# Optimization experiments

Hardware: AMD Instinct MI355X
Metric: run time of the kernel (lower is better)

The kernel has to match this reference:

```python
import jax, jax.numpy as jnp
import numpy as np

K = 3   # spatial_kernel_size
M = 5   # memory_size


def setup_inputs() -> dict:
    key = jax.random.key(0)
    ks = jax.random.split(key, 16)
    C = 64
    B, H, D, W = 2, 24, 24, 24
    s = 0.05
    n = jax.random.normal
    return {
        "x": n(ks[0], (B, C, H, D, W), jnp.float32),
        "prev_memory": jnp.zeros((B, C), jnp.float32),
        "Wq": n(ks[1], (C, C), jnp.float32) * s,
        "bq": n(ks[2], (C,), jnp.float32) * s,
        "Wk": n(ks[3], (C, C), jnp.float32) * s,
        "bk": n(ks[4], (C,), jnp.float32) * s,
        "Wv": n(ks[5], (C, C), jnp.float32) * s,
        "bv": n(ks[6], (C,), jnp.float32) * s,
        "mem_key": n(ks[7], (C, M), jnp.float32),
        "mem_value": n(ks[8], (C, M), jnp.float32),
        "Wg": n(ks[9], (C, 2 * C), jnp.float32) * s,
        "bg": n(ks[10], (C,), jnp.float32) * s,
        "W_ih": n(ks[11], (3 * C, C), jnp.float32) * s,
        "W_hh": n(ks[12], (3 * C, C), jnp.float32) * s,
        "b_ih": n(ks[13], (3 * C,), jnp.float32) * s,
        "b_hh": n(ks[14], (3 * C,), jnp.float32) * s,
    }


def _patches(x, k):
    # x: (B,C,H,D,W) -> (B,C,k^3,H,D,W) local neighborhoods (zero-padded)
    B, C, H, D, W = x.shape
    p = k // 2
    xp = jnp.pad(x, ((0, 0), (0, 0), (p, p), (p, p), (p, p)))
    sl = [xp[:, :, i:i + H, j:j + D, l:l + W]
          for i in range(k) for j in range(k) for l in range(k)]
    return jnp.stack(sl, axis=2)


def reference(x, prev_memory, Wq, bq, Wk, bk, Wv, bv, mem_key, mem_value,
              Wg, bg, W_ih, W_hh, b_ih, b_hh):
    B, C, H, D, W = x.shape
    N = H * D * W
    xf = x.reshape(B, C, N)
    pf = _patches(x, K).reshape(B, C, K ** 3, N)

    # 1x1x1 conv projections (pure channel mixes)
    q = jnp.einsum('oc,bcn->bon', Wq, xf) + bq[None, :, None]            # (B,C,N)
    k_sp = jnp.einsum('oc,bcmn->bomn', Wk, pf) + bk[None, :, None, None]  # (B,C,27,N)
    v_sp = jnp.einsum('oc,bcmn->bomn', Wv, pf) + bv[None, :, None, None]

    # memory tokens broadcast over all spatial locations
    k_mem = jnp.broadcast_to(mem_key[None, :, :, None], (B, C, M, N))
    v_mem = jnp.broadcast_to(mem_value[None, :, :, None], (B, C, M, N))
    kk = jnp.concatenate([k_mem, k_sp], axis=2)   # (B,C,M+27,N)
    vv = jnp.concatenate([v_mem, v_sp], axis=2)

    # per-channel scalar attention over memory+neighborhood axis
    attn = jax.nn.softmax(q[:, :, None, :] * kk / jnp.sqrt(jnp.float32(C)), axis=2)
    out = jnp.sum(attn * vv, axis=2).reshape(B, C, H, D, W)

    # sigmoid gate over concat([x, out])
    gin = jnp.concatenate([xf, out.reshape(B, C, N)], axis=1)  # (B,2C,N)
    gate = jax.nn.sigmoid(jnp.einsum('oc,bcn->bon', Wg, gin)
                          + bg[None, :, None]).reshape(B, C, H, D, W)
    out = gate * out + (1.0 - gate) * x

    # GRU memory update on spatially pooled features (torch GRUCell math)
    mu = out.mean(axis=(2, 3, 4))                 # (B,C)
    gi = mu @ W_ih.T + b_ih
    gh = prev_memory @ W_hh.T + b_hh
    ir, iz, ii = jnp.split(gi, 3, axis=1)
    hr, hz, hn = jnp.split(gh, 3, axis=1)
    r = jax.nn.sigmoid(ir + hr)
    z = jax.nn.sigmoid(iz + hz)
    ng = jnp.tanh(ii + r * hn)
    new_memory = (1.0 - z) * ng + z * prev_memory
    return out, new_memory
```

## Files before the change

### kernel.cpp

```cpp
#include <hip/hip_runtime.h>
#include <math.h>

#define NPOS 13824
#define CDIM 64
#define BTCH 2
#define LOG2E 1.4426950408889634f
#define QSCALE (0.125f * LOG2E)

__device__ __forceinline__ unsigned int f2bf1(float f) {
  unsigned int u = __float_as_uint(f);
  return (u + 0x7FFFu + ((u >> 16) & 1u)) >> 16;
}

__global__ __launch_bounds__(256) void qkvg_kernel(
    const float* __restrict__ x,
    const float* __restrict__ Wq, const float* __restrict__ bq,
    const float* __restrict__ Wk, const float* __restrict__ bk,
    const float* __restrict__ Wv, const float* __restrict__ bv,
    const float* __restrict__ Wg,
    float* __restrict__ Qb, float* __restrict__ Kb, float* __restrict__ Vb,
    float* __restrict__ GXT, float* __restrict__ pool)
{
  __shared__ __align__(16) float wqt[64*68];
  __shared__ __align__(16) float wkt[64*68];
  __shared__ __align__(16) float wvt[64*68];
  __shared__ __align__(16) float wgt[64*68];
  const int t  = threadIdx.x;
  const int bi = blockIdx.x;
  const int b  = bi / 216;
  const int n0 = (bi - b*216) * 64;
  if (bi == 0 && t < 128) pool[t] = 0.0f;

  #pragma unroll
  for (int k = 0; k < 16; ++k) {
    int idx = t + k*256;
    int lo = idx & 63, hi = idx >> 6;
    wqt[lo*68 + hi] = Wq[idx] * QSCALE;
    wkt[lo*68 + hi] = Wk[idx];
    wvt[lo*68 + hi] = Wv[idx];
    wgt[lo*68 + hi] = Wg[hi*128 + lo];
  }
  __syncthreads();

  const int c0  = (t & 15) * 4;
  const int nn0 = (t >> 4) * 4;
  const float* xbase = x + (size_t)(b*64)*NPOS + n0 + nn0;
  float aq[4][4] = {}; float ak[4][4] = {}; float av[4][4] = {}; float ag[4][4] = {};
  #pragma unroll 4
  for (int cp = 0; cp < 64; ++cp) {
    const float4 xv4 = *(const float4*)(xbase + (size_t)cp*NPOS);
    const float4 q4  = *(const float4*)&wqt[cp*68 + c0];
    const float4 k4  = *(const float4*)&wkt[cp*68 + c0];
    const float4 v4  = *(const float4*)&wvt[cp*68 + c0];
    const float4 g4  = *(const float4*)&wgt[cp*68 + c0];
    const float xa[4] = {xv4.x, xv4.y, xv4.z, xv4.w};
    const float qa[4] = {q4.x, q4.y, q4.z, q4.w};
    const float ka[4] = {k4.x, k4.y, k4.z, k4.w};
    const float va[4] = {v4.x, v4.y, v4.z, v4.w};
    const float ga[4] = {g4.x, g4.y, g4.z, g4.w};
    #pragma unroll
    for (int ci = 0; ci < 4; ++ci)
      #pragma unroll
      for (int ni = 0; ni < 4; ++ni) {
        aq[ci][ni] = fmaf(qa[ci], xa[ni], aq[ci][ni]);
        ak[ci][ni] = fmaf(ka[ci], xa[ni], ak[ci][ni]);
        av[ci][ni] = fmaf(va[ci], xa[ni], av[ci][ni]);
        ag[ci][ni] = fmaf(ga[ci], xa[ni], ag[ci][ni]);
      }
  }
  float4 xr[4];
  #pragma unroll
  for (int e = 0; e < 4; ++e)
    xr[e] = *(const float4*)(x + (size_t)(b*64 + c0 + e)*NPOS + n0 + nn0);
  const float xre[4][4] = {{xr[0].x,xr[0].y,xr[0].z,xr[0].w},
                           {xr[1].x,xr[1].y,xr[1].z,xr[1].w},
                           {xr[2].x,xr[2].y,xr[2].z,xr[2].w},
                           {xr[3].x,xr[3].y,xr[3].z,xr[3].w}};
  const float4 bq4 = *(const float4*)&bq[c0];
  const float4 bk4 = *(const float4*)&bk[c0];
  const float4 bv4 = *(const float4*)&bv[c0];
  #pragma unroll
  for (int ni = 0; ni < 4; ++ni) {
    const int p = b*NPOS + n0 + nn0 + ni;
    float4 o;
    o = make_float4(fmaf(bq4.x,QSCALE,aq[0][ni]), fmaf(bq4.y,QSCALE,aq[1][ni]),
                    fmaf(bq4.z,QSCALE,aq[2][ni]), fmaf(bq4.w,QSCALE,aq[3][ni]));
    *(float4*)&Qb[p*64 + c0] = o;
    o = make_float4(ak[0][ni]+bk4.x, ak[1][ni]+bk4.y, ak[2][ni]+bk4.z, ak[3][ni]+bk4.w);
    *(float4*)&Kb[p*64 + c0] = o;
    o = make_float4(av[0][ni]+bv4.x, av[1][ni]+bv4.y, av[2][ni]+bv4.z, av[3][ni]+bv4.w);
    *(float4*)&Vb[p*64 + c0] = o;
    o = make_float4(ag[0][ni], xre[0][ni], ag[1][ni], xre[1][ni]);
    *(float4*)&GXT[(size_t)(p*64 + c0)*2]     = o;
    o = make_float4(ag[2][ni], xre[2][ni], ag[3][ni], xre[3][ni]);
    *(float4*)&GXT[(size_t)(p*64 + c0)*2 + 4] = o;
  }
}

__global__ __launch_bounds__(256, 4) void attn_kernel(
    float* __restrict__ QOT,
    const float* __restrict__ Kb, const float* __restrict__ Vb,
    const float* __restrict__ GXT,
    const float* __restrict__ bk, const float* __restrict__ bv,
    const float* __restrict__ memk, const float* __restrict__ memv,
    const float* __restrict__ Wg, const float* __restrict__ bg,
    float* __restrict__ pool)
{
  __shared__ __align__(16) unsigned int kvbuf[8000];
  __shared__ __align__(16) float als[256];
  const int t = threadIdx.x;
  const int c = t & 63;
  const int w = t >> 6;

  {
    float* wgt2 = (float*)kvbuf;
    #pragma unroll
    for (int k = 0; k < 16; ++k) {
      int u = t + k*256;
      int cp = u >> 6, j = u & 63;
      wgt2[j*65 + cp] = Wg[cp*128 + 64 + j];
    }
  }
  __syncthreads();
  unsigned int wg2p[32];
  {
    const float* wgt2 = (const float*)kvbuf;
    #pragma unroll
    for (int j2 = 0; j2 < 32; ++j2) {
      unsigned lo = f2bf1(wgt2[(2*j2)*65 + c]);
      unsigned hi = f2bf1(wgt2[(2*j2+1)*65 + c]);
      wg2p[j2] = lo | (hi << 16);
    }
  }
  float mk[5], mv[5];
  #pragma unroll
  for (int m = 0; m < 5; ++m) { mk[m] = memk[c*5 + m]; mv[m] = memv[c*5 + m]; }
  const float bg_c = bg[c];
  __syncthreads();

  const int bi = (int)(blockIdx.x & 7) * 128 + (int)(blockIdx.x >> 3);
  const int b  = bi >> 9;
  const int tb = bi & 511;
  const int h0 = (tb >> 6) * 3;
  const int d0 = ((tb >> 3) & 7) * 3;
  const int w0 = (tb & 7) * 3;
  const int bN = b * NPOS;

  for (int u = t; u < 125*16; u += 256) {
    int pos = u >> 4, q4 = u & 15;
    int ph = pos / 25, pr = pos - ph*25;
    int pd = pr / 5,  pw = pr - pd*5;
    int hh = h0 - 1 + ph, dd = d0 - 1 + pd, ww = w0 - 1 + pw;
    bool inb = ((unsigned)hh < 24u) && ((unsigned)dd < 24u) && ((unsigned)ww < 24u);
    float4 kf, vf;
    if (inb) {
      const size_t off = ((size_t)(bN + hh*576 + dd*24 + ww))*64 + q4*4;
      kf = *(const float4*)(Kb + off);
      vf = *(const float4*)(Vb + off);
    } else {
      kf = ((const float4*)bk)[q4];
      vf = ((const float4*)bv)[q4];
    }
    uint4 pk;
    pk.x = (f2bf1(kf.x) << 16) | f2bf1(vf.x);
    pk.y = (f2bf1(kf.y) << 16) | f2bf1(vf.y);
    pk.z = (f2bf1(kf.z) << 16) | f2bf1(vf.z);
    pk.w = (f2bf1(kf.w) << 16) | f2bf1(vf.w);
    *(uint4*)&kvbuf[pos*64 + q4*4] = pk;
  }
  __syncthreads();

  float pacc = 0.0f;
  int li = w;
  int lh = li / 9, lr = li - lh*9, ld = lr / 3, lw = lr - ld*3;
  int p  = bN + (h0+lh)*576 + (d0+ld)*24 + (w0+lw);
  int hb = (lh*25 + ld*5 + lw)*64 + c;
  float q2 = QOT[p*64 + c];
  for (; li < 27; li += 4) {
    const int li_n = li + 4;
    int p_n = p, hb_n = hb;
    if (li_n < 27) {
      const int lh2 = li_n / 9, lr2 = li_n - lh2*9;
      const int ld2 = lr2 / 3,  lw2 = lr2 - ld2*3;
      p_n  = bN + (h0+lh2)*576 + (d0+ld2)*24 + (w0+lw2);
      hb_n = (lh2*25 + ld2*5 + lw2)*64 + c;
    }
    const float q_n = QOT[p_n*64 + c];
    const float2 gx = *(const float2*)&GXT[(size_t)(p*64 + c)*2];

    const unsigned int* kvp = &kvbuf[hb];
    unsigned int kvreg[27];
    #pragma unroll
    for (int i = 0; i < 3; ++i)
      #pragma unroll
      for (int j = 0; j < 3; ++j)
        #pragma unroll
        for (int l = 0; l < 3; ++l)
          kvreg[i*9 + j*3 + l] = kvp[(i*25 + j*5 + l)*64];
    float mx0 = q2*mk[0], mx1 = q2*mk[1], mx2 = q2*mk[2], mx3 = q2*mk[3];
    mx0 = fmaxf(mx0, q2*mk[4]);
    #pragma unroll
    for (int s = 0; s < 27; ++s) {
      float kf = __uint_as_float(kvreg[s] & 0xFFFF0000u);
      float lv = q2 * kf;
      if ((s & 3) == 0) mx0 = fmaxf(mx0, lv);
      else if ((s & 3) == 1) mx1 = fmaxf(mx1, lv);
      else if ((s & 3) == 2) mx2 = fmaxf(mx2, lv);
      else mx3 = fmaxf(mx3, lv);
    }
    const float maxv = fmaxf(fmaxf(mx0, mx1), fmaxf(mx2, mx3));

    float s0 = 0.f, s1 = 0.f, o0 = 0.f, o1 = 0.f;
    #pragma unroll
    for (int m = 0; m < 5; ++m) {
      float pf = __builtin_amdgcn_exp2f(fmaf(q2, mk[m], -maxv));
      if (m & 1) { s1 += pf; o1 = fmaf(pf, mv[m], o1); }
      else       { s0 += pf; o0 = fmaf(pf, mv[m], o0); }
    }
    #pragma unroll
    for (int s = 0; s < 27; ++s) {
      unsigned int kv = kvreg[s];
      float kf = __uint_as_float(kv & 0xFFFF0000u);
      float vf = __uint_as_float(kv << 16);
      float pf = __builtin_amdgcn_exp2f(fmaf(q2, kf, -maxv));
      if (s & 1) { s1 += pf; o1 = fmaf(pf, vf, o1); }
      else       { s0 += pf; o0 = fmaf(pf, vf, o0); }
    }
    const float att = (o0 + o1) * __builtin_amdgcn_rcpf(s0 + s1);

    als[w*64 + c] = att;
    float g0 = gx.x + bg_c, g1 = 0.f, g2 = 0.f, g3 = 0.f;
    #pragma unroll
    for (int j4 = 0; j4 < 16; ++j4) {
      const float4 a4 = *(const float4*)&als[w*64 + j4*4];
      const unsigned pk0 = wg2p[2*j4], pk1 = wg2p[2*j4+1];
      g0 = fmaf(__uint_as_float(pk0 << 16),         a4.x, g0);
      g1 = fmaf(__uint_as_float(pk0 & 0xFFFF0000u), a4.y, g1);
      g2 = fmaf(__uint_as_float(pk1 << 16),         a4.z, g2);
      g3 = fmaf(__uint_as_float(pk1 & 0xFFFF0000u), a4.w, g3);
    }
    const float gl   = (g0 + g1) + (g2 + g3);
    const float gate = __builtin_amdgcn_rcpf(1.0f + __builtin_amdgcn_exp2f(-LOG2E * gl));
    const float fin  = fmaf(gate, att - gx.y, gx.y);
    QOT[p*64 + c] = fin;
    pacc += fin;

    p = p_n; hb = hb_n; q2 = q_n;
  }

  als[t] = pacc;
  __syncthreads();
  if (t < 64) {
    float s = als[t] + als[64 + t] + als[128 + t] + als[192 + t];
    atomicAdd(&pool[b*64 + t], s);
  }
}

__global__ __launch_bounds__(256) void outpool_kernel(
    const float* __restrict__ OT, float* __restrict__ out,
    const float* __restrict__ pool, const float* __restrict__ prev,
    const float* __restrict__ W_ih, const float* __restrict__ W_hh,
    const float* __restrict__ b_ih, const float* __restrict__ b_hh,
    float* __restrict__ outmem)
{
  __shared__ __align__(16) float ls[64*65];
  __shared__ __align__(16) float mu[128];
  __shared__ float gi[384];
  __shared__ float gh[384];
  const int t  = threadIdx.x;
  const int bi = blockIdx.x;
  const int b  = bi / 216;
  const int n0 = (bi - b*216) * 64;
  #pragma unroll
  for (int i = 0; i < 16; ++i) {
    int u = i*256 + t;
    int pos = u >> 6, cc = u & 63;
    ls[cc*65 + pos] = OT[(size_t)(b*NPOS + n0 + pos)*64 + cc];
  }
  if (bi == 0 && t < 128) mu[t] = pool[t] * (1.0f / (float)NPOS);
  __syncthreads();
  #pragma unroll
  for (int i = 0; i < 16; ++i) {
    int u = i*256 + t;
    int cc = u >> 6, j = u & 63;
    out[(size_t)(b*64 + cc)*NPOS + n0 + j] = ls[cc*65 + j];
  }
  if (bi != 0) return;

  for (int r = t; r < 384; r += 256) {
    const int b2 = r / 192, j = r - b2*192;
    const float4* wi4 = (const float4*)(W_ih + (size_t)j*64);
    const float4* wh4 = (const float4*)(W_hh + (size_t)j*64);
    const float4* mu4 = (const float4*)(mu + b2*64);
    const float4* pv4 = (const float4*)(prev + b2*64);
    float sgi = b_ih[j], sgh = b_hh[j];
    #pragma unroll
    for (int k = 0; k < 16; ++k) {
      float4 wv = wi4[k], m4 = mu4[k];
      sgi = fmaf(wv.x, m4.x, sgi); sgi = fmaf(wv.y, m4.y, sgi);
      sgi = fmaf(wv.z, m4.z, sgi); sgi = fmaf(wv.w, m4.w, sgi);
      float4 hv = wh4[k], p4 = pv4[k];
      sgh = fmaf(hv.x, p4.x, sgh); sgh = fmaf(hv.y, p4.y, sgh);
      sgh = fmaf(hv.z, p4.z, sgh); sgh = fmaf(hv.w, p4.w, sgh);
    }
    gi[r] = sgi; gh[r] = sgh;
  }
  __syncthreads();
  if (t < 128) {
    const int b2 = t >> 6, cc = t & 63;
    float ir = gi[b2*192 + cc],       hr = gh[b2*192 + cc];
    float iz = gi[b2*192 + 64 + cc],  hz = gh[b2*192 + 64 + cc];
    float ii = gi[b2*192 + 128 + cc], hn = gh[b2*192 + 128 + cc];
    float rr = 1.0f / (1.0f + __builtin_amdgcn_exp2f(-LOG2E * (ir + hr)));
    float zz = 1.0f / (1.0f + __builtin_amdgcn_exp2f(-LOG2E * (iz + hz)));
    float ng = tanhf(ii + rr * hn);
    outmem[t] = (1.0f - zz) * ng + zz * prev[t];
  }
}

extern "C" void kernel_launch(void* const* d_in, const int* in_sizes, int n_in,
                              void* d_out, int out_size, void* d_ws, size_t ws_size,
                              hipStream_t stream) {
  const float* x    = (const float*)d_in[0];
  const float* prev = (const float*)d_in[1];
  const float* Wq   = (const float*)d_in[2];
  const float* bq   = (const float*)d_in[3];
  const float* Wk   = (const float*)d_in[4];
  const float* bk   = (const float*)d_in[5];
  const float* Wv   = (const float*)d_in[6];
  const float* bv   = (const float*)d_in[7];
  const float* memk = (const float*)d_in[8];
  const float* memv = (const float*)d_in[9];
  const float* Wg   = (const float*)d_in[10];
  const float* bg   = (const float*)d_in[11];
  const float* W_ih = (const float*)d_in[12];
  const float* W_hh = (const float*)d_in[13];
  const float* b_ih = (const float*)d_in[14];
  const float* b_hh = (const float*)d_in[15];

  float* out    = (float*)d_out;
  float* outmem = out + (size_t)BTCH*CDIM*NPOS;

  const size_t SZ = (size_t)BTCH*NPOS*CDIM;
  float* wsf  = (float*)d_ws;
  float* Qb   = wsf;
  float* Kb   = wsf + SZ;
  float* Vb   = wsf + 2*SZ;
  float* GXT  = wsf + 3*SZ;
  float* pool = wsf + 5*SZ;

  qkvg_kernel<<<BTCH*216, 256, 0, stream>>>(x, Wq, bq, Wk, bk, Wv, bv, Wg,
                                            Qb, Kb, Vb, GXT, pool);
  attn_kernel<<<BTCH*512, 256, 0, stream>>>(Qb, Kb, Vb, GXT,
                                            bk, bv, memk, memv, Wg, bg, pool);
  outpool_kernel<<<BTCH*216, 256, 0, stream>>>(Qb, out, pool, prev,
                                               W_ih, W_hh, b_ih, b_hh, outmem);
}
```

Before: 169.4 us.

## Store packed bf16 K/V from projection, drop softmax max pass, process two positions per iteration

The projection kernel now writes K and V as one packed bf16 buffer instead of two fp32 buffers, which halves the intermediate write traffic and the attention kernel's halo loads. The attention kernel no longer computes a running max before the exponentials, which relies on the scaled logits staying small enough not to overflow. Each thread now handles two output positions per loop iteration, interleaving their exp and gate work for more instruction-level parallelism. The cost is higher register pressure and a possible loss of numerical safety for large logits.

```diff
diff --git a/kernel.cpp b/kernel.cpp
--- a/kernel.cpp
+++ b/kernel.cpp
@@ -18,7 +18,7 @@
     const float* __restrict__ Wk, const float* __restrict__ bk,
     const float* __restrict__ Wv, const float* __restrict__ bv,
     const float* __restrict__ Wg,
-    float* __restrict__ Qb, float* __restrict__ Kb, float* __restrict__ Vb,
+    float* __restrict__ Qb, unsigned int* __restrict__ KVp,
     float* __restrict__ GXT, float* __restrict__ pool)
 {
   __shared__ __align__(16) float wqt[64*68];
@@ -86,10 +86,12 @@
     o = make_float4(fmaf(bq4.x,QSCALE,aq[0][ni]), fmaf(bq4.y,QSCALE,aq[1][ni]),
                     fmaf(bq4.z,QSCALE,aq[2][ni]), fmaf(bq4.w,QSCALE,aq[3][ni]));
     *(float4*)&Qb[p*64 + c0] = o;
-    o = make_float4(ak[0][ni]+bk4.x, ak[1][ni]+bk4.y, ak[2][ni]+bk4.z, ak[3][ni]+bk4.w);
-    *(float4*)&Kb[p*64 + c0] = o;
-    o = make_float4(av[0][ni]+bv4.x, av[1][ni]+bv4.y, av[2][ni]+bv4.z, av[3][ni]+bv4.w);
-    *(float4*)&Vb[p*64 + c0] = o;
+    uint4 kv;
+    kv.x = (f2bf1(ak[0][ni]+bk4.x) << 16) | f2bf1(av[0][ni]+bv4.x);
+    kv.y = (f2bf1(ak[1][ni]+bk4.y) << 16) | f2bf1(av[1][ni]+bv4.y);
+    kv.z = (f2bf1(ak[2][ni]+bk4.z) << 16) | f2bf1(av[2][ni]+bv4.z);
+    kv.w = (f2bf1(ak[3][ni]+bk4.w) << 16) | f2bf1(av[3][ni]+bv4.w);
+    *(uint4*)&KVp[p*64 + c0] = kv;
     o = make_float4(ag[0][ni], xre[0][ni], ag[1][ni], xre[1][ni]);
     *(float4*)&GXT[(size_t)(p*64 + c0)*2]     = o;
     o = make_float4(ag[2][ni], xre[2][ni], ag[3][ni], xre[3][ni]);
@@ -99,7 +101,7 @@
 
 __global__ __launch_bounds__(256, 4) void attn_kernel(
     float* __restrict__ QOT,
-    const float* __restrict__ Kb, const float* __restrict__ Vb,
+    const unsigned int* __restrict__ KVp,
     const float* __restrict__ GXT,
     const float* __restrict__ bk, const float* __restrict__ bv,
     const float* __restrict__ memk, const float* __restrict__ memv,
@@ -107,7 +109,8 @@
     float* __restrict__ pool)
 {
   __shared__ __align__(16) unsigned int kvbuf[8000];
-  __shared__ __align__(16) float als[256];
+  __shared__ __align__(16) float alsA[256];
+  __shared__ __align__(16) float alsB[256];
   const int t = threadIdx.x;
   const int c = t & 63;
   const int w = t >> 6;
@@ -152,106 +155,110 @@
     int pd = pr / 5,  pw = pr - pd*5;
     int hh = h0 - 1 + ph, dd = d0 - 1 + pd, ww = w0 - 1 + pw;
     bool inb = ((unsigned)hh < 24u) && ((unsigned)dd < 24u) && ((unsigned)ww < 24u);
-    float4 kf, vf;
+    uint4 kv;
     if (inb) {
-      const size_t off = ((size_t)(bN + hh*576 + dd*24 + ww))*64 + q4*4;
-      kf = *(const float4*)(Kb + off);
-      vf = *(const float4*)(Vb + off);
+      kv = *(const uint4*)(KVp + ((size_t)(bN + hh*576 + dd*24 + ww))*64 + q4*4);
     } else {
-      kf = ((const float4*)bk)[q4];
-      vf = ((const float4*)bv)[q4];
-    }
-    uint4 pk;
-    pk.x = (f2bf1(kf.x) << 16) | f2bf1(vf.x);
-    pk.y = (f2bf1(kf.y) << 16) | f2bf1(vf.y);
-    pk.z = (f2bf1(kf.z) << 16) | f2bf1(vf.z);
-    pk.w = (f2bf1(kf.w) << 16) | f2bf1(vf.w);
-    *(uint4*)&kvbuf[pos*64 + q4*4] = pk;
+      const float4 kf = ((const float4*)bk)[q4];
+      const float4 vf = ((const float4*)bv)[q4];
+      kv.x = (f2bf1(kf.x) << 16) | f2bf1(vf.x);
+      kv.y = (f2bf1(kf.y) << 16) | f2bf1(vf.y);
+      kv.z = (f2bf1(kf.z) << 16) | f2bf1(vf.z);
+      kv.w = (f2bf1(kf.w) << 16) | f2bf1(vf.w);
+    }
+    *(uint4*)&kvbuf[pos*64 + q4*4] = kv;
   }
   __syncthreads();
 
   float pacc = 0.0f;
-  int li = w;
-  int lh = li / 9, lr = li - lh*9, ld = lr / 3, lw = lr - ld*3;
-  int p  = bN + (h0+lh)*576 + (d0+ld)*24 + (w0+lw);
-  int hb = (lh*25 + ld*5 + lw)*64 + c;
-  float q2 = QOT[p*64 + c];
-  for (; li < 27; li += 4) {
-    const int li_n = li + 4;
-    int p_n = p, hb_n = hb;
-    if (li_n < 27) {
-      const int lh2 = li_n / 9, lr2 = li_n - lh2*9;
-      const int ld2 = lr2 / 3,  lw2 = lr2 - ld2*3;
-      p_n  = bN + (h0+lh2)*576 + (d0+ld2)*24 + (w0+lw2);
-      hb_n = (lh2*25 + ld2*5 + lw2)*64 + c;
-    }
-    const float q_n = QOT[p_n*64 + c];
-    const float2 gx = *(const float2*)&GXT[(size_t)(p*64 + c)*2];
-
-    const unsigned int* kvp = &kvbuf[hb];
-    unsigned int kvreg[27];
+  for (int li = w; li < 27; li += 8) {
+    const int liB0 = li + 4;
+    const bool hasB = liB0 < 27;
+    const int liB = hasB ? liB0 : li;
+
+    const int lhA = li / 9,  lrA = li - lhA*9;
+    const int ldA = lrA / 3, lwA = lrA - ldA*3;
+    const int pA  = bN + (h0+lhA)*576 + (d0+ldA)*24 + (w0+lwA);
+    const int hbA = (lhA*25 + ldA*5 + lwA)*64 + c;
+    const int lhB = liB / 9,  lrB = liB - lhB*9;
+    const int ldB = lrB / 3,  lwB = lrB - ldB*3;
+    const int pB  = bN + (h0+lhB)*576 + (d0+ldB)*24 + (w0+lwB);
+    const int hbB = (lhB*25 + ldB*5 + lwB)*64 + c;
+
+    const float qA = QOT[pA*64 + c];
+    const float qB = QOT[pB*64 + c];
+    const float2 gxA = *(const float2*)&GXT[(size_t)(pA*64 + c)*2];
+    const float2 gxB = *(const float2*)&GXT[(size_t)(pB*64 + c)*2];
+
+    float sA0 = 0.f, sA1 = 0.f, oA0 = 0.f, oA1 = 0.f;
+    float sB0 = 0.f, sB1 = 0.f, oB0 = 0.f, oB1 = 0.f;
+    #pragma unroll
+    for (int m = 0; m < 5; ++m) {
+      const float pfA = __builtin_amdgcn_exp2f(qA * mk[m]);
+      const float pfB = __builtin_amdgcn_exp2f(qB * mk[m]);
+      if (m & 1) { sA1 += pfA; oA1 = fmaf(pfA, mv[m], oA1);
+                   sB1 += pfB; oB1 = fmaf(pfB, mv[m], oB1); }
+      else       { sA0 += pfA; oA0 = fmaf(pfA, mv[m], oA0);
+                   sB0 += pfB; oB0 = fmaf(pfB, mv[m], oB0); }
+    }
+    const unsigned int* kvA = &kvbuf[hbA];
+    const unsigned int* kvB = &kvbuf[hbB];
     #pragma unroll
     for (int i = 0; i < 3; ++i)
       #pragma unroll
       for (int j = 0; j < 3; ++j)
         #pragma unroll
-        for (int l = 0; l < 3; ++l)
-          kvreg[i*9 + j*3 + l] = kvp[(i*25 + j*5 + l)*64];
-    float mx0 = q2*mk[0], mx1 = q2*mk[1], mx2 = q2*mk[2], mx3 = q2*mk[3];
-    mx0 = fmaxf(mx0, q2*mk[4]);
-    #pragma unroll
-    for (int s = 0; s < 27; ++s) {
-      float kf = __uint_as_float(kvreg[s] & 0xFFFF0000u);
-      float lv = q2 * kf;
-      if ((s & 3) == 0) mx0 = fmaxf(mx0, lv);
-      else if ((s & 3) == 1) mx1 = fmaxf(mx1, lv);
-      else if ((s & 3) == 2) mx2 = fmaxf(mx2, lv);
-      else mx3 = fmaxf(mx3, lv);
-    }
-    const float maxv = fmaxf(fmaxf(mx0, mx1), fmaxf(mx2, mx3));
-
-    float s0 = 0.f, s1 = 0.f, o0 = 0.f, o1 = 0.f;
-    #pragma unroll
-    for (int m = 0; m < 5; ++m) {
-      float pf = __builtin_amdgcn_exp2f(fmaf(q2, mk[m], -maxv));
-      if (m & 1) { s1 += pf; o1 = fmaf(pf, mv[m], o1); }
-      else       { s0 += pf; o0 = fmaf(pf, mv[m], o0); }
-    }
-    #pragma unroll
-    for (int s = 0; s < 27; ++s) {
-      unsigned int kv = kvreg[s];
-      float kf = __uint_as_float(kv & 0xFFFF0000u);
-      float vf = __uint_as_float(kv << 16);
-      float pf = __builtin_amdgcn_exp2f(fmaf(q2, kf, -maxv));
-      if (s & 1) { s1 += pf; o1 = fmaf(pf, vf, o1); }
-      else       { s0 += pf; o0 = fmaf(pf, vf, o0); }
-    }
-    const float att = (o0 + o1) * __builtin_amdgcn_rcpf(s0 + s1);
-
-    als[w*64 + c] = att;
-    float g0 = gx.x + bg_c, g1 = 0.f, g2 = 0.f, g3 = 0.f;
+        for (int l = 0; l < 3; ++l) {
+          const int s4  = i*9 + j*3 + l;
+          const int off = (i*25 + j*5 + l)*64;
+          const unsigned a = kvA[off], bb2 = kvB[off];
+          const float kA = __uint_as_float(a & 0xFFFF0000u);
+          const float vA = __uint_as_float(a << 16);
+          const float kB = __uint_as_float(bb2 & 0xFFFF0000u);
+          const float vB = __uint_as_float(bb2 << 16);
+          const float pfA = __builtin_amdgcn_exp2f(qA * kA);
+          const float pfB = __builtin_amdgcn_exp2f(qB * kB);
+          if (s4 & 1) { sA1 += pfA; oA1 = fmaf(pfA, vA, oA1);
+                        sB1 += pfB; oB1 = fmaf(pfB, vB, oB1); }
+          else        { sA0 += pfA; oA0 = fmaf(pfA, vA, oA0);
+                        sB0 += pfB; oB0 = fmaf(pfB, vB, oB0); }
+        }
+    const float attA = (oA0 + oA1) * __builtin_amdgcn_rcpf(sA0 + sA1);
+    const float attB = (oB0 + oB1) * __builtin_amdgcn_rcpf(sB0 + sB1);
+
+    alsA[w*64 + c] = attA;
+    alsB[w*64 + c] = attB;
+    float gA0 = gxA.x + bg_c, gA1 = 0.f, gA2 = 0.f, gA3 = 0.f;
+    float gB0 = gxB.x + bg_c, gB1 = 0.f, gB2 = 0.f, gB3 = 0.f;
     #pragma unroll
     for (int j4 = 0; j4 < 16; ++j4) {
-      const float4 a4 = *(const float4*)&als[w*64 + j4*4];
+      const float4 a4 = *(const float4*)&alsA[w*64 + j4*4];
+      const float4 b4 = *(const float4*)&alsB[w*64 + j4*4];
       const unsigned pk0 = wg2p[2*j4], pk1 = wg2p[2*j4+1];
-      g0 = fmaf(__uint_as_float(pk0 << 16),         a4.x, g0);
-      g1 = fmaf(__uint_as_float(pk0 & 0xFFFF0000u), a4.y, g1);
-      g2 = fmaf(__uint_as_float(pk1 << 16),         a4.z, g2);
-      g3 = fmaf(__uint_as_float(pk1 & 0xFFFF0000u), a4.w, g3);
-    }
-    const float gl   = (g0 + g1) + (g2 + g3);
-    const float gate = __builtin_amdgcn_rcpf(1.0f + __builtin_amdgcn_exp2f(-LOG2E * gl));
-    const float fin  = fmaf(gate, att - gx.y, gx.y);
-    QOT[p*64 + c] = fin;
-    pacc += fin;
-
-    p = p_n; hb = hb_n; q2 = q_n;
-  }
-
-  als[t] = pacc;
+      const float w0f = __uint_as_float(pk0 << 16);
+      const float w1f = __uint_as_float(pk0 & 0xFFFF0000u);
+      const float w2f = __uint_as_float(pk1 << 16);
+      const float w3f = __uint_as_float(pk1 & 0xFFFF0000u);
+      gA0 = fmaf(w0f, a4.x, gA0); gB0 = fmaf(w0f, b4.x, gB0);
+      gA1 = fmaf(w1f, a4.y, gA1); gB1 = fmaf(w1f, b4.y, gB1);
+      gA2 = fmaf(w2f, a4.z, gA2); gB2 = fmaf(w2f, b4.z, gB2);
+      gA3 = fmaf(w3f, a4.w, gA3); gB3 = fmaf(w3f, b4.w, gB3);
+    }
+    const float glA   = (gA0 + gA1) + (gA2 + gA3);
+    const float glB   = (gB0 + gB1) + (gB2 + gB3);
+    const float gateA = __builtin_amdgcn_rcpf(1.0f + __builtin_amdgcn_exp2f(-LOG2E * glA));
+    const float gateB = __builtin_amdgcn_rcpf(1.0f + __builtin_amdgcn_exp2f(-LOG2E * glB));
+    const float finA  = fmaf(gateA, attA - gxA.y, gxA.y);
+    const float finB  = fmaf(gateB, attB - gxB.y, gxB.y);
+    QOT[pA*64 + c] = finA;
+    pacc += finA;
+    if (hasB) { QOT[pB*64 + c] = finB; pacc += finB; }
+  }
+
+  alsA[t] = pacc;
   __syncthreads();
   if (t < 64) {
-    float s = als[t] + als[64 + t] + als[128 + t] + als[192 + t];
+    float s = alsA[t] + alsA[64 + t] + alsA[128 + t] + alsA[192 + t];
     atomicAdd(&pool[b*64 + t], s);
   }
 }
@@ -342,16 +349,15 @@
   float* outmem = out + (size_t)BTCH*CDIM*NPOS;
 
   const size_t SZ = (size_t)BTCH*NPOS*CDIM;
-  float* wsf  = (float*)d_ws;
-  float* Qb   = wsf;
-  float* Kb   = wsf + SZ;
-  float* Vb   = wsf + 2*SZ;
-  float* GXT  = wsf + 3*SZ;
-  float* pool = wsf + 5*SZ;
+  float* wsf       = (float*)d_ws;
+  float* Qb        = wsf;
+  unsigned int* KVp = (unsigned int*)(wsf + SZ);
+  float* GXT       = wsf + 2*SZ;
+  float* pool      = wsf + 4*SZ;
 
   qkvg_kernel<<<BTCH*216, 256, 0, stream>>>(x, Wq, bq, Wk, bk, Wv, bv, Wg,
-                                            Qb, Kb, Vb, GXT, pool);
-  attn_kernel<<<BTCH*512, 256, 0, stream>>>(Qb, Kb, Vb, GXT,
+                                            Qb, KVp, GXT, pool);
+  attn_kernel<<<BTCH*512, 256, 0, stream>>>(Qb, KVp, GXT,
                                             bk, bv, memk, memv, Wg, bg, pool);
   outpool_kernel<<<BTCH*216, 256, 0, stream>>>(Qb, out, pool, prev,
                                                W_ih, W_hh, b_ih, b_hh, outmem);
```

Measured after the change: 150.2 us. 1.13x faster.
